# Performance work log

Hardware: AMD Instinct MI355X
Metric: run time of the kernel (lower is better)

Reference implementation:

```python
import jax, jax.numpy as jnp
import numpy as np

B, S, I, H = 128, 1024, 512, 1024


def setup_inputs() -> dict:
    key = jax.random.key(0)
    k0, k1, k2 = jax.random.split(key, 3)
    scale = 0.02
    return {
        "x": jax.random.normal(k0, (B, S, I), jnp.float32),
        "feature_weighting": jnp.ones((1, 1, I), jnp.float32),
        "temporal_weighting": jnp.ones((1, S, 1), jnp.float32),
        "magnitude": jnp.ones((1,), jnp.float32),
        "W0": jax.random.normal(k1, (3 * H, I + H), jnp.float32) * scale,
        "b0": jnp.zeros((3 * H,), jnp.float32),
        "W1": jax.random.normal(k2, (3 * H, 2 * H), jnp.float32) * scale,
        "b1": jnp.zeros((3 * H,), jnp.float32),
    }


def _cell(x_t, h_prev, c_prev, W, b):
    # gates: [B, 3H] from cat(x, h_prev) @ W.T + b
    gates = jnp.concatenate([x_t, h_prev], axis=1) @ W.T + b
    i, g, o = jnp.split(gates, 3, axis=1)
    f = jax.nn.sigmoid(c_prev)            # note: forget gate from c_prev (module's quirk)
    c_new = f * c_prev + jax.nn.sigmoid(i) * jnp.tanh(g)
    h_new = jax.nn.sigmoid(o) * jnp.tanh(c_new) * f  # extra *f (module's quirk)
    return h_new, c_new


def reference(x, feature_weighting, temporal_weighting, magnitude, W0, b0, W1, b1):
    batch = x.shape[0]
    hid = W0.shape[0] // 3
    x = x * feature_weighting * temporal_weighting * jnp.exp(magnitude)
    zeros = jnp.zeros((batch, hid), x.dtype)
    init = (zeros, zeros, zeros, zeros)  # h0, c0, h1, c1

    def step(carry, x_t):
        h0, c0, h1, c1 = carry
        h0, c0 = _cell(x_t, h0, c0, W0, b0)
        h1, c1 = _cell(h0, h1, c1, W1, b1)
        return (h0, c0, h1, c1), h1

    (h0, c0, h1, c1), ys = jax.lax.scan(step, init, jnp.swapaxes(x, 0, 1))
    outputs = jnp.swapaxes(ys, 0, 1)  # [B, S, H]
    return outputs, ((h0, c0), (h1, c1))
```

## Files before the change

kernel.cpp:

```cpp
#include <hip/hip_runtime.h>
#include <hip/hip_bf16.h>


typedef __attribute__((ext_vector_type(8))) _Float16 f16x8;
typedef __attribute__((ext_vector_type(4))) float f32x4;
typedef unsigned long long u64;
#define DEV __device__ __forceinline__

namespace {
constexpr int Bb = 128, Ss = 1024, Ii = 512, Hh = 1024;
constexpr int K0 = Ii + Hh;
constexpr int K1 = 2 * Hh;
constexpr int NWG = 256;
constexpr int NPH = Ss + 1;
constexpr int RING = 16;
constexpr int SSTR = 32;

constexpr size_t BH    = (size_t)Bb * Hh;
constexpr size_t OF_H0 = (size_t)Bb * Ss * Hh;
constexpr size_t OF_C0 = OF_H0 + BH;
constexpr size_t OF_H1 = OF_C0 + BH;
constexpr size_t OF_C1 = OF_H1 + BH;

constexpr size_t WS_SLOTS = 4096;
constexpr size_t WS_C0    = 40960;
constexpr size_t WS_C1    = WS_C0 + BH * 4;
constexpr size_t RINGF    = (size_t)RING * BH * 2;
constexpr size_t WS_H0F   = WS_C1 + BH * 4;
constexpr size_t WS_H1F   = WS_H0F + RINGF;
constexpr size_t WS_ZEND  = WS_H1F + RINGF;
constexpr size_t WSZ_W0   = (size_t)3 * Hh * K0 * 2;
constexpr size_t WSZ_W1   = (size_t)3 * Hh * K1 * 2;
constexpr size_t WS_W0F   = WS_ZEND;
constexpr size_t WS_W1F   = WS_W0F + WSZ_W0;
constexpr size_t WS_NEED  = WS_W1F + WSZ_W1;

constexpr int CHUNKB    = 3072;
constexpr int LO_BYTES  = 48 * CHUNKB;
constexpr int RED_BYTES = 4 * 3 * 64 * 16;
constexpr int DYN_LDS   = LO_BYTES + RED_BYTES;
}

DEV unsigned short f16b(float f) {
  return __builtin_bit_cast(unsigned short, (_Float16)f);
}
DEV float sig_(float x) { return 1.f / (1.f + __expf(-x)); }
DEV float tanh_(float x) {
  float e = __expf(-2.f * fabsf(x));
  return copysignf((1.f - e) / (1.f + e), x);
}
DEV f16x8 ldh(const unsigned short* p) { return *reinterpret_cast<const f16x8*>(p); }
#define MFMAH __builtin_amdgcn_mfma_f32_16x16x32_f16

__global__ void k_zero(uint4* p, int n16) {
  for (int i = blockIdx.x * blockDim.x + threadIdx.x; i < n16; i += gridDim.x * blockDim.x)
    p[i] = make_uint4(0u, 0u, 0u, 0u);
}

__global__ void k_convert(const float* __restrict__ W0, const float* __restrict__ W1,
                          unsigned short* __restrict__ w0f, unsigned short* __restrict__ w1f) {
  const long NW04 = (long)3 * Hh * K0 / 4;
  const long NW14 = (long)3 * Hh * K1 / 4;
  const long total = NW04 + NW14;
  for (long i = (long)blockIdx.x * blockDim.x + threadIdx.x; i < total;
       i += (long)gridDim.x * blockDim.x) {
    long e; const float* src; unsigned short* dst;
    if (i < NW04) { e = i * 4;          src = W0 + e; dst = w0f + e; }
    else          { e = (i - NW04) * 4; src = W1 + e; dst = w1f + e; }
    f32x4 v = *(const f32x4*)src;
    u64 pk = 0;
#pragma unroll
    for (int e2 = 0; e2 < 4; ++e2) pk |= (u64)f16b(v[e2]) << (16 * e2);
    *(u64*)dst = pk;
  }
}

#define LD_W(g, kl)                                                           \
  (*(const f16x8*)(lds + ((kl) >> 5) * CHUNKB + (g) * 1024 + l4 * 256 + l15 * 16))

#define HLOAD(arr, n, hP, kaB)                                                \
  _Pragma("unroll") for (int c_ = 0; c_ < (n); ++c_)                          \
    arr[c_] = ldh((hP) + (kaB) + c_ * 32);

#define HCOMP(arr, n, koB)                                                    \
  _Pragma("unroll") for (int c_ = 0; c_ < (n); ++c_) {                        \
    const int ko_ = (koB) + c_ * 32;                                          \
    f32x4 &I_ = (c_ & 1) ? aI1 : aI0;                                         \
    f32x4 &G_ = (c_ & 1) ? aG1 : aG0;                                         \
    f32x4 &O_ = (c_ & 1) ? aO1 : aO0;                                         \
    I_ = MFMAH(LD_W(0, ko_), arr[c_], I_, 0, 0, 0);                           \
    G_ = MFMAH(LD_W(1, ko_), arr[c_], G_, 0, 0, 0);                           \
    O_ = MFMAH(LD_W(2, ko_), arr[c_], O_, 0, 0, 0);                           \
  }

#define WLOAD(a0, a1, a2, n, koB)                                             \
  _Pragma("unroll") for (int c_ = 0; c_ < (n); ++c_) {                        \
    const int ko_ = (koB) + c_ * 32;                                          \
    a0[c_] = ldh(wf + off0 + ko_);                                            \
    a1[c_] = ldh(wf + off1 + ko_);                                            \
    a2[c_] = ldh(wf + off2 + ko_);                                            \
  }

#define GCOMP(h_, a0, a1, a2, n)                                              \
  _Pragma("unroll") for (int c_ = 0; c_ < (n); ++c_) {                        \
    f32x4 &I_ = (c_ & 1) ? aI1 : aI0;                                         \
    f32x4 &G_ = (c_ & 1) ? aG1 : aG0;                                         \
    f32x4 &O_ = (c_ & 1) ? aO1 : aO0;                                         \
    I_ = MFMAH(a0[c_], h_[c_], I_, 0, 0, 0);                                  \
    G_ = MFMAH(a1[c_], h_[c_], G_, 0, 0, 0);                                  \
    O_ = MFMAH(a2[c_], h_[c_], O_, 0, 0, 0);                                  \
  }

#define XCOMP()                                                               \
  _Pragma("unroll") for (int c_ = 0; c_ < 16; ++c_) {                         \
    const int ko_ = c_ * 32;                                                  \
    f32x4 &I_ = (c_ & 1) ? aI1 : aI0;                                         \
    f32x4 &G_ = (c_ & 1) ? aG1 : aG0;                                         \
    f32x4 &O_ = (c_ & 1) ? aO1 : aO0;                                         \
    I_ = MFMAH(LD_W(0, ko_), xp[c_], I_, 0, 0, 0);                            \
    G_ = MFMAH(LD_W(1, ko_), xp[c_], G_, 0, 0, 0);                            \
    O_ = MFMAH(LD_W(2, ko_), xp[c_], O_, 0, 0, 0);                            \
  }

#define XPREF(tn)                                                             \
  do {                                                                        \
    const float* pxn_ = xf + ((size_t)bact * Ss + (tn)) * Ii + l4 * 8;        \
    const float twn_ = tw[tn] * emag;                                         \
    _Pragma("unroll") for (int c_ = 0; c_ < 16; ++c_) {                       \
      const int k_ = c_ * 32;                                                 \
      f32x4 a0_ = *(const f32x4*)(pxn_ + k_);                                 \
      f32x4 a1_ = *(const f32x4*)(pxn_ + k_ + 4);                             \
      f32x4 b0_ = *(const f32x4*)(fw + k_ + l4 * 8);                          \
      f32x4 b1_ = *(const f32x4*)(fw + k_ + l4 * 8 + 4);                      \
      a0_ *= b0_ * twn_; a1_ *= b1_ * twn_;                                   \
      _Pragma("unroll") for (int e_ = 0; e_ < 4; ++e_) {                      \
        xp[c_][e_] = (_Float16)a0_[e_];                                       \
        xp[c_][e_ + 4] = (_Float16)a1_[e_];                                   \
      }                                                                       \
    }                                                                         \
  } while (0)

#define ZACC() do { f32x4 z_ = {0.f,0.f,0.f,0.f};                             \
    aI0 = z_; aG0 = z_; aO0 = z_; aI1 = z_; aG1 = z_; aO1 = z_; } while (0)

__global__ __launch_bounds__(512, 1) void lstm_persist(
    const float* __restrict__ xf,
    const float* __restrict__ fw, const float* __restrict__ tw, const float* __restrict__ mag,
    const unsigned short* __restrict__ w0f, const float* __restrict__ b0,
    const unsigned short* __restrict__ w1f, const float* __restrict__ b1,
    float* __restrict__ out,
    unsigned short* __restrict__ h0f, unsigned short* __restrict__ h1f,
    float* __restrict__ c0, float* __restrict__ c1,
    int* __restrict__ slots) {
  extern __shared__ char lds[];
  f32x4* red = reinterpret_cast<f32x4*>(lds + LO_BYTES);

  const int tid = threadIdx.x;
  const int lane = tid & 63;
  const int wv = tid >> 6;
  const int mt = wv & 3;
  const int kh = wv >> 2;
  const int l15 = lane & 15, l4 = lane >> 4;

  const int wg = blockIdx.x;
  const int layer = wg >> 7;
  const int i = wg & 127;
  const int x8 = i & 7;
  const int kk = i >> 3;
  const int mg = x8 >> 2;
  const int jt = (x8 & 3) * 16 + kk;
  const int jb = jt * 16;

  const int bact = mg * 64 + mt * 16 + l15;
  const int j0 = jb + l4 * 4;
  const bool xwave = (layer == 0) && (kh == 0);

  const int K = layer ? K1 : K0;
  const unsigned short* wf = layer ? w1f : w0f;
  const size_t off0 = (size_t)(0 * Hh + jb + l15) * K + l4 * 8;
  const size_t off1 = (size_t)(1 * Hh + jb + l15) * K + l4 * 8;
  const size_t off2 = (size_t)(2 * Hh + jb + l15) * K + l4 * 8;

  const float* bb = layer ? b1 : b0;
  const f32x4 bi = *(const f32x4*)(bb + j0);
  const f32x4 bg = *(const f32x4*)(bb + Hh + j0);
  const f32x4 bo = *(const f32x4*)(bb + 2 * Hh + j0);

  float* cst = (layer ? c1 : c0) + (size_t)bact * Hh + j0;
  float* outb = out + (size_t)bact * Ss * Hh + j0;
  const float emag = __expf(mag[0]);

  {
    const u64* wsl = (const u64*)wf;
    const int K4 = K >> 2;
    for (int idx = tid; idx < 48 * 384; idx += 512) {
      int R = idx / 384;
      int o = idx - R * 384;
      int g = R >> 4, rr = R & 15;
      u64 v = wsl[(size_t)(g * Hh + jb + rr) * K4 + o];
      *(u64*)(lds + (o >> 3) * CHUNKB + g * 1024 + ((o >> 1) & 3) * 256 +
              rr * 16 + (o & 1) * 8) = v;
    }
  }
  __syncthreads();

  f32x4 aI0, aG0, aO0, aI1, aG1, aO1;
  ZACC();
  f16x8 xp[16];
  if (xwave) { XPREF(0); XCOMP(); }

  for (int p = 0; p < NPH; ++p) {
    const bool act = layer ? (p >= 1) : (p < Ss);
    const int t = layer ? (p - 1) : p;
    const int rslot = (p - 1) & (RING - 1);
    const int wslot = p & (RING - 1);

    if (act) {
      if (!xwave) ZACC();
      const unsigned short* h0r = h0f + (size_t)rslot * BH + (size_t)bact * Hh + l4 * 8;
      const unsigned short* h1r = h1f + (size_t)rslot * BH + (size_t)bact * Hh + l4 * 8;

      if (layer == 0) {
        if (kh == 0) {
          f16x8 hA[8], hB[8];
          HLOAD(hA, 8, h0r, 0);
          HLOAD(hB, 8, h0r, 256);
          HCOMP(hA, 8, Ii);
          HCOMP(hB, 8, Ii + 256);
        } else {
          f16x8 hA[8], hB[8];
          HLOAD(hA, 8, h0r, 512);
          HLOAD(hB, 8, h0r, 768);
          HCOMP(hA, 8, Ii + 512);
          HCOMP(hB, 8, Ii + 768);
        }
      } else {
        if (kh == 0) {
          f16x8 g0[12], g1[12], g2a[8], g2b[4], g3[12];
          HLOAD(g0, 12, h0r, 0);
          HLOAD(g1, 12, h0r, 384);
          HCOMP(g0, 12, 0);
          HLOAD(g2a, 8, h0r, 768);
          HLOAD(g2b, 4, h1r, 0);
          HCOMP(g1, 12, 384);
          HLOAD(g3, 12, h1r, 128);
          HCOMP(g2a, 8, 768);
          HCOMP(g2b, 4, Hh);
          HCOMP(g3, 12, Hh + 128);
        } else {
          {
            f16x8 sh[6], sA[6], sB[6], sC[6];
            HLOAD(sh, 6, h1r, 512);
            WLOAD(sA, sB, sC, 6, Hh + 512);
            GCOMP(sh, sA, sB, sC, 6);
          }
          {
            f16x8 sh[6], sA[6], sB[6], sC[6];
            HLOAD(sh, 6, h1r, 704);
            WLOAD(sA, sB, sC, 6, Hh + 704);
            GCOMP(sh, sA, sB, sC, 6);
          }
          {
            f16x8 sh[4], sA[4], sB[4], sC[4];
            HLOAD(sh, 4, h1r, 896);
            WLOAD(sA, sB, sC, 4, Hh + 896);
            GCOMP(sh, sA, sB, sC, 4);
          }
        }
      }

      if (kh == 1) {
        red[((mt * 3 + 0) << 6) + lane] = aI0 + aI1;
        red[((mt * 3 + 1) << 6) + lane] = aG0 + aG1;
        red[((mt * 3 + 2) << 6) + lane] = aO0 + aO1;
      }
      __syncthreads();
      if (kh == 0) {
        f32x4 ai = aI0 + aI1 + red[((mt * 3 + 0) << 6) + lane] + bi;
        f32x4 ag = aG0 + aG1 + red[((mt * 3 + 1) << 6) + lane] + bg;
        f32x4 ao = aO0 + aO1 + red[((mt * 3 + 2) << 6) + lane] + bo;
        f32x4 cp = *(const f32x4*)cst;
        f32x4 cn, hn;
        u64 hpk = 0;
#pragma unroll
        for (int r = 0; r < 4; ++r) {
          float f = sig_(cp[r]);
          float cc = f * cp[r] + sig_(ai[r]) * tanh_(ag[r]);
          float hh = sig_(ao[r]) * tanh_(cc) * f;
          cn[r] = cc; hn[r] = hh;
          hpk |= (u64)f16b(hh) << (16 * r);
        }
        *(f32x4*)cst = cn;
        const size_t wbase = (size_t)wslot * BH + (size_t)bact * Hh + j0;
        __hip_atomic_store((u64*)((layer ? h1f : h0f) + wbase), hpk,
                           __ATOMIC_RELAXED, __HIP_MEMORY_SCOPE_AGENT);
        if (layer) {
          *(f32x4*)(outb + (size_t)t * Hh) = hn;
          if (t == Ss - 1) {
            *(f32x4*)(out + OF_H1 + (size_t)bact * Hh + j0) = hn;
            *(f32x4*)(out + OF_C1 + (size_t)bact * Hh + j0) = cn;
          }
        } else if (t == Ss - 1) {
          *(f32x4*)(out + OF_H0 + (size_t)bact * Hh + j0) = hn;
          *(f32x4*)(out + OF_C0 + (size_t)bact * Hh + j0) = cn;
        }
      }
      if (xwave && t + 1 < Ss) {
        XPREF(t + 1);
        ZACC();
        XCOMP();
      }
    }

    if (p < NPH - 1) {
      __syncthreads();
      if (tid == 0)
        __hip_atomic_store(&slots[wg * SSTR], p + 1, __ATOMIC_RELAXED,
                           __HIP_MEMORY_SCOPE_AGENT);
      bool ok = (tid >= 256);
      int gd = 0;
      do {
        if (!ok)
          ok = __hip_atomic_load(&slots[tid * SSTR], __ATOMIC_RELAXED,
                                 __HIP_MEMORY_SCOPE_AGENT) > p;
        if (!ok) __builtin_amdgcn_s_sleep(1);
      } while (!__syncthreads_and(ok) && ++gd < (1 << 22));
      if ((p & (RING - 1)) == (RING - 1)) {
        if (tid == 0) __builtin_amdgcn_fence(__ATOMIC_ACQUIRE, "agent");
        __syncthreads();
      }
    }
  }
}

extern "C" void kernel_launch(void* const* d_in, const int* in_sizes, int n_in,
                              void* d_out, int out_size, void* d_ws, size_t ws_size,
                              hipStream_t stream) {
  const float* x   = (const float*)d_in[0];
  const float* fw  = (const float*)d_in[1];
  const float* tw  = (const float*)d_in[2];
  const float* mag = (const float*)d_in[3];
  const float* W0  = (const float*)d_in[4];
  const float* b0  = (const float*)d_in[5];
  const float* W1  = (const float*)d_in[6];
  const float* b1  = (const float*)d_in[7];
  float* out = (float*)d_out;
  char* ws = (char*)d_ws;

  if (ws_size < WS_NEED) return;

  unsigned short* w0f = (unsigned short*)(ws + WS_W0F);
  unsigned short* w1f = (unsigned short*)(ws + WS_W1F);

  (void)hipFuncSetAttribute((const void*)lstm_persist,
                            hipFuncAttributeMaxDynamicSharedMemorySize, DYN_LDS);

  k_zero<<<2048, 256, 0, stream>>>((uint4*)ws, (int)(WS_ZEND / 16));
  k_convert<<<1024, 256, 0, stream>>>(W0, W1, w0f, w1f);

  lstm_persist<<<NWG, 512, DYN_LDS, stream>>>(
      x, fw, tw, mag, w0f, b0, w1f, b1, out,
      (unsigned short*)(ws + WS_H0F), (unsigned short*)(ws + WS_H1F),
      (float*)(ws + WS_C0), (float*)(ws + WS_C1),
      (int*)(ws + WS_SLOTS));
}
```

Before: 17.26 ms.

## Replace global barrier with per-domain dependency waits and layer lag

Replaces the all-256-workgroup barrier each phase with targeted waits. Each workgroup now waits only on the 64 workgroups of its own batch-half and layer, plus the producer/consumer domain of the other layer. Layer 0 may run up to LAG steps ahead of layer 1, bounded by the ring size. The x-projection MFMA is also moved from the end of the step into the h-dependent compute, leaving only the x prefetch after the step. This cuts global synchronization latency, but ring-slot reuse safety now depends on LAG being smaller than RING and on the acquire fence placement.

```diff
diff --git a/kernel.cpp b/kernel.cpp
--- a/kernel.cpp
+++ b/kernel.cpp
@@ -14,6 +14,7 @@
 constexpr int NWG = 256;
 constexpr int NPH = Ss + 1;
 constexpr int RING = 16;
+constexpr int LAG  = 12;
 constexpr int SSTR = 32;
 
 constexpr size_t BH    = (size_t)Bb * Hh;
@@ -140,9 +141,6 @@
     }                                                                         \
   } while (0)
 
-#define ZACC() do { f32x4 z_ = {0.f,0.f,0.f,0.f};                             \
-    aI0 = z_; aG0 = z_; aO0 = z_; aI1 = z_; aG1 = z_; aO1 = z_; } while (0)
-
 __global__ __launch_bounds__(512, 1) void lstm_persist(
     const float* __restrict__ xf,
     const float* __restrict__ fw, const float* __restrict__ tw, const float* __restrict__ mag,
@@ -171,6 +169,10 @@
   const int jt = (x8 & 3) * 16 + kk;
   const int jb = jt * 16;
 
+  const int dom  = layer * 2 + mg;
+  const int pdom = layer ? mg : 2 + mg;
+  const int idx  = (x8 & 3) * 16 + kk;
+
   const int bact = mg * 64 + mt * 16 + l15;
   const int j0 = jb + l4 * 4;
   const bool xwave = (layer == 0) && (kh == 0);
@@ -193,21 +195,18 @@
   {
     const u64* wsl = (const u64*)wf;
     const int K4 = K >> 2;
-    for (int idx = tid; idx < 48 * 384; idx += 512) {
-      int R = idx / 384;
-      int o = idx - R * 384;
+    for (int idx2 = tid; idx2 < 48 * 384; idx2 += 512) {
+      int R = idx2 / 384;
+      int o = idx2 - R * 384;
       int g = R >> 4, rr = R & 15;
       u64 v = wsl[(size_t)(g * Hh + jb + rr) * K4 + o];
       *(u64*)(lds + (o >> 3) * CHUNKB + g * 1024 + ((o >> 1) & 3) * 256 +
               rr * 16 + (o & 1) * 8) = v;
     }
   }
+  f16x8 xp[16];
+  if (xwave) XPREF(0);
   __syncthreads();
-
-  f32x4 aI0, aG0, aO0, aI1, aG1, aO1;
-  ZACC();
-  f16x8 xp[16];
-  if (xwave) { XPREF(0); XCOMP(); }
 
   for (int p = 0; p < NPH; ++p) {
     const bool act = layer ? (p >= 1) : (p < Ss);
@@ -216,7 +215,8 @@
     const int wslot = p & (RING - 1);
 
     if (act) {
-      if (!xwave) ZACC();
+      f32x4 z = {0.f, 0.f, 0.f, 0.f};
+      f32x4 aI0 = z, aG0 = z, aO0 = z, aI1 = z, aG1 = z, aO1 = z;
       const unsigned short* h0r = h0f + (size_t)rslot * BH + (size_t)bact * Hh + l4 * 8;
       const unsigned short* h1r = h1f + (size_t)rslot * BH + (size_t)bact * Hh + l4 * 8;
 
@@ -225,6 +225,7 @@
           f16x8 hA[8], hB[8];
           HLOAD(hA, 8, h0r, 0);
           HLOAD(hB, 8, h0r, 256);
+          XCOMP();
           HCOMP(hA, 8, Ii);
           HCOMP(hB, 8, Ii + 256);
         } else {
@@ -305,24 +306,29 @@
           *(f32x4*)(out + OF_C0 + (size_t)bact * Hh + j0) = cn;
         }
       }
-      if (xwave && t + 1 < Ss) {
-        XPREF(t + 1);
-        ZACC();
-        XCOMP();
-      }
+      if (xwave && t + 1 < Ss) XPREF(t + 1);
     }
 
     if (p < NPH - 1) {
       __syncthreads();
       if (tid == 0)
-        __hip_atomic_store(&slots[wg * SSTR], p + 1, __ATOMIC_RELAXED,
-                           __HIP_MEMORY_SCOPE_AGENT);
-      bool ok = (tid >= 256);
+        __hip_atomic_store(&slots[(dom * 64 + idx) * SSTR], p + 1,
+                           __ATOMIC_RELAXED, __HIP_MEMORY_SCOPE_AGENT);
+      const int pthr = layer ? (p + 1) : (p + 1 - LAG);
+      bool ok;
+      if (tid < 64)        ok = false;
+      else if (tid < 128)  ok = (pthr <= 0);
+      else                 ok = true;
       int gd = 0;
       do {
-        if (!ok)
-          ok = __hip_atomic_load(&slots[tid * SSTR], __ATOMIC_RELAXED,
-                                 __HIP_MEMORY_SCOPE_AGENT) > p;
+        if (!ok) {
+          int v = (tid < 64)
+              ? __hip_atomic_load(&slots[(dom * 64 + tid) * SSTR],
+                                  __ATOMIC_RELAXED, __HIP_MEMORY_SCOPE_AGENT)
+              : __hip_atomic_load(&slots[(pdom * 64 + (tid - 64)) * SSTR],
+                                  __ATOMIC_RELAXED, __HIP_MEMORY_SCOPE_AGENT);
+          ok = v >= ((tid < 64) ? (p + 1) : pthr);
+        }
         if (!ok) __builtin_amdgcn_s_sleep(1);
       } while (!__syncthreads_and(ok) && ++gd < (1 << 22));
       if ((p & (RING - 1)) == (RING - 1)) {
```

New measurement: 16.10 ms. 6.7% less time.
